# Kernel optimization log

Measured on AMD Instinct MI355X. Metric: run time of the kernel, lower is better.

The kernel has to match this reference:

```python
import jax, jax.numpy as jnp
import numpy as np

N_NODES = 50000
N_EDGES = 640000
WIDTH = 128
K = 5
N_CONVS = 6  # 1 input + 4 hidden + 1 output ChebConv layers


def setup_inputs() -> dict:
    key = jax.random.key(0)
    k1, k2, k3, k4 = jax.random.split(key, 4)
    scale = 1.0 / np.sqrt(WIDTH)
    x = jax.random.normal(k1, (N_NODES, WIDTH), dtype=jnp.float32)
    edge_index = jax.random.randint(k2, (2, N_EDGES), 0, N_NODES, dtype=jnp.int64)
    conv_w = jax.random.normal(k3, (N_CONVS, K, WIDTH, WIDTH), dtype=jnp.float32) * scale
    conv_b = jnp.zeros((N_CONVS, WIDTH), dtype=jnp.float32)
    lin_w = jax.random.normal(k4, (WIDTH, 1), dtype=jnp.float32) * scale
    lin_b = jnp.zeros((1,), dtype=jnp.float32)
    return {"x": x, "edge_index": edge_index, "conv_w": conv_w,
            "conv_b": conv_b, "lin_w": lin_w, "lin_b": lin_b}


def _cheb_norm(edge_index):
    # PyG ChebConv with normalization='sym', lambda_max=2.0:
    # L_hat = 2/lambda_max * (I - D^-1/2 A D^-1/2) - I = -D^-1/2 A D^-1/2
    # (diagonal terms cancel), so per-edge weight = -d_i^-1/2 * d_j^-1/2.
    src, dst = edge_index[0], edge_index[1]
    ones = jnp.ones((edge_index.shape[1],), dtype=jnp.float32)
    deg = jax.ops.segment_sum(ones, dst, num_segments=N_NODES)
    d_inv_sqrt = jnp.where(deg > 0, jax.lax.rsqrt(jnp.maximum(deg, 1e-12)), 0.0)
    return -d_inv_sqrt[src] * d_inv_sqrt[dst]


def _propagate(x, src, dst, norm):
    # L_hat @ x via gather -> weight -> scatter-add
    msg = norm[:, None] * x[src]              # [E, C]
    return jax.ops.segment_sum(msg, dst, num_segments=N_NODES)


def _cheb_conv(x, W, b, src, dst, norm):
    # Chebyshev recurrence: T0=x, T1=Lx, Tk = 2*L*T(k-1) - T(k-2)
    Tx0 = x
    out = Tx0 @ W[0]
    Tx1 = _propagate(Tx0, src, dst, norm)
    out = out + Tx1 @ W[1]
    for k in range(2, K):
        Tx2 = 2.0 * _propagate(Tx1, src, dst, norm) - Tx0
        out = out + Tx2 @ W[k]
        Tx0, Tx1 = Tx1, Tx2
    return out + b


def reference(x, edge_index, conv_w, conv_b, lin_w, lin_b):
    src, dst = edge_index[0], edge_index[1]
    norm = _cheb_norm(edge_index)
    h = x
    # first 5 convs followed by ReLU (dropout is identity in eval mode)
    for l in range(N_CONVS - 1):
        h = _cheb_conv(h, conv_w[l], conv_b[l], src, dst, norm)
        h = jax.nn.relu(h)
    # final conv (no activation) + Linear(128, 1)
    h = _cheb_conv(h, conv_w[N_CONVS - 1], conv_b[N_CONVS - 1], src, dst, norm)
    return h @ lin_w + lin_b
```

## Files before the change

### kernel.cpp

```cpp
#include <hip/hip_runtime.h>


#define NN 50000
#define NE 640000
#define WID 128
#define PROP_BLOCKS 2048

typedef __attribute__((ext_vector_type(8))) short bf16x8;
typedef __attribute__((ext_vector_type(4))) float f32x4;

__device__ __forceinline__ unsigned short f2bf(float f) {
  union { float f; unsigned int u; } v; v.f = f;
  unsigned int r = v.u + 0x7FFF + ((v.u >> 16) & 1);
  return (unsigned short)(r >> 16);
}
__device__ __forceinline__ unsigned int pack2(float lo, float hi) {
  return (unsigned int)f2bf(lo) | ((unsigned int)f2bf(hi) << 16);
}
__device__ __forceinline__ float bflo(unsigned int u) {
  return __uint_as_float(u << 16);
}
__device__ __forceinline__ float bfhi(unsigned int u) {
  return __uint_as_float(u & 0xffff0000u);
}
__device__ __forceinline__ float dec_norm(unsigned int p) {
  unsigned int lo = p & 0xfffu;
  float v = -__uint_as_float(((112u + ((p >> 8) & 15u)) << 23) | ((p & 255u) << 15));
  return (lo == 0u) ? 0.f : v;
}


__global__ __launch_bounds__(256) void degree_kernel(const int* __restrict__ ei,
                                                     int* __restrict__ deg, int E) {
  int e = blockIdx.x * 256 + threadIdx.x;
  if (e < E) atomicAdd(&deg[ei[E + e]], 1);
}

__global__ __launch_bounds__(256) void scan1_kernel(const int* __restrict__ deg,
                                                    int* __restrict__ lex,
                                                    int* __restrict__ bsum,
                                                    float* __restrict__ dinv, int n) {
  __shared__ int ws[4];
  int tid = threadIdx.x, lane = tid & 63, w = tid >> 6;
  int i = blockIdx.x * 256 + tid;
  int cnt = (i < n) ? deg[i] : 0;
  if (i < n) {
    float d = (float)cnt;
    dinv[i] = d > 0.0f ? rsqrtf(d) : 0.0f;
  }
  int v = cnt;
#pragma unroll
  for (int off = 1; off < 64; off <<= 1) {
    int u = __shfl_up(v, off, 64);
    if (lane >= off) v += u;
  }
  if (lane == 63) ws[w] = v;
  __syncthreads();
  int wexcl = 0;
#pragma unroll
  for (int k = 0; k < 4; ++k) wexcl += (k < w) ? ws[k] : 0;
  if (i < n) lex[i] = wexcl + v - cnt;
  if (tid == 255) bsum[blockIdx.x] = wexcl + v;
}

__global__ __launch_bounds__(256) void scan2_kernel(const int* __restrict__ bsum,
                                                    int* __restrict__ boff,
                                                    int* __restrict__ row_end, int nb) {
  __shared__ int ws[4];
  int tid = threadIdx.x, lane = tid & 63, w = tid >> 6;
  int cnt = (tid < nb) ? bsum[tid] : 0;
  int v = cnt;
#pragma unroll
  for (int off = 1; off < 64; off <<= 1) {
    int u = __shfl_up(v, off, 64);
    if (lane >= off) v += u;
  }
  if (lane == 63) ws[w] = v;
  __syncthreads();
  int wexcl = 0;
#pragma unroll
  for (int k = 0; k < 4; ++k) wexcl += (k < w) ? ws[k] : 0;
  if (tid < nb) boff[tid] = wexcl + v - cnt;
  if (tid == 255) *row_end = wexcl + v;
}

__global__ __launch_bounds__(256) void scan3_kernel(const int* __restrict__ lex,
                                                    const int* __restrict__ boff,
                                                    int* __restrict__ row_start,
                                                    int* __restrict__ fill_ptr, int n) {
  int i = blockIdx.x * 256 + threadIdx.x;
  if (i < n) {
    int rs = lex[i] + boff[blockIdx.x];
    row_start[i] = rs;
    fill_ptr[i] = rs;
  }
}

__global__ __launch_bounds__(256) void fill_kernel(const int* __restrict__ ei,
                                                   const float* __restrict__ dinv,
                                                   int* __restrict__ fill_ptr,
                                                   unsigned int* __restrict__ csr, int E) {
  int e = blockIdx.x * 256 + threadIdx.x;
  if (e < E) {
    int s = ei[e];
    int d = ei[E + e];
    int pos = atomicAdd(&fill_ptr[d], 1);
    float mag = dinv[s] * dinv[d];
    unsigned int bits = __float_as_uint(mag);
    unsigned int pk = (unsigned int)s << 12;
    if (bits != 0u) {
      bits += 0x4000u;
      int ex = (int)((bits >> 23) & 255u) - 112;
      ex = max(0, min(15, ex));
      pk |= ((unsigned int)ex << 8) | ((bits >> 15) & 0xffu);
    }
    csr[pos] = pk;
  }
}

__global__ __launch_bounds__(256) void cvt_kernel(const float* __restrict__ x,
                                                  unsigned short* __restrict__ xo,
                                                  const float* __restrict__ w,
                                                  unsigned short* __restrict__ wt,
                                                  int nx, int nw) {
  int i = blockIdx.x * 256 + threadIdx.x;
  if (i < nx) {
    xo[i] = f2bf(x[i]);
  } else if (i < nx + nw) {
    int j = i - nx;
    int l = j / (WID * 640);
    int r = j % (WID * 640);
    int col = r / 640;
    int k = r % 640;
    int kk = k >> 7, m = k & 127;
    wt[j] = f2bf(w[(((size_t)l * 5 + kk) * WID + m) * WID + col]);
  }
}

__global__ __launch_bounds__(256) void vk_kernel(const float* __restrict__ w,
                                                 const float* __restrict__ b,
                                                 const float* __restrict__ lw,
                                                 const float* __restrict__ lb,
                                                 float* __restrict__ V,
                                                 float* __restrict__ cst) {
  int idx = blockIdx.x * 256 + threadIdx.x;
  if (idx < 5 * WID) {
    int k = idx / WID, i = idx % WID;
    const float4* wr = (const float4*)(w + (((size_t)5 * 5 + k) * WID + i) * WID);
    const float4* l4 = (const float4*)lw;
    float s = 0.f;
#pragma unroll 8
    for (int j = 0; j < WID / 4; ++j) {
      float4 a = wr[j], c = l4[j];
      s += a.x * c.x + a.y * c.y + a.z * c.z + a.w * c.w;
    }
    V[idx] = s;
  }
  if (blockIdx.x == 0 && threadIdx.x == 0) {
    float s = 0.f;
    for (int c = 0; c < WID; ++c) s += b[5 * WID + c] * lw[c];
    *cst = s + lb[0];
  }
}


__global__ __launch_bounds__(256) void prop_kernel(unsigned short* __restrict__ out,
                                                   const unsigned short* __restrict__ xin,
                                                   const unsigned short* __restrict__ sub,
                                                   float scale,
                                                   const int* __restrict__ row_start,
                                                   const unsigned int* __restrict__ csr,
                                                   int n) {
  int t = threadIdx.x & 15;
  for (int node = blockIdx.x * 16 + (threadIdx.x >> 4); node < n;
       node += PROP_BLOCKS * 16) {
    int s = row_start[node], e = row_start[node + 1];
    float a0 = 0.f, a1 = 0.f, a2 = 0.f, a3 = 0.f;
    float a4 = 0.f, a5 = 0.f, a6 = 0.f, a7 = 0.f;
    for (int base = s; base < e; base += 16) {
      int cnt = min(16, e - base);
      unsigned int ed = (t < cnt) ? csr[base + t] : 0u;
      int j = 0;
      for (; j + 4 <= cnt; j += 4) {
        unsigned int p0 = (unsigned int)__shfl((int)ed, j, 16);
        unsigned int p1 = (unsigned int)__shfl((int)ed, j + 1, 16);
        unsigned int p2 = (unsigned int)__shfl((int)ed, j + 2, 16);
        unsigned int p3 = (unsigned int)__shfl((int)ed, j + 3, 16);
        int s0 = p0 >> 12, s1 = p1 >> 12, s2 = p2 >> 12, s3 = p3 >> 12;
        float n0 = dec_norm(p0), n1 = dec_norm(p1), n2 = dec_norm(p2), n3 = dec_norm(p3);
        const uint4 v0 = *(const uint4*)(xin + (size_t)s0 * WID + t * 8);
        const uint4 v1 = *(const uint4*)(xin + (size_t)s1 * WID + t * 8);
        const uint4 v2 = *(const uint4*)(xin + (size_t)s2 * WID + t * 8);
        const uint4 v3 = *(const uint4*)(xin + (size_t)s3 * WID + t * 8);
        a0 += n0 * bflo(v0.x) + n1 * bflo(v1.x) + n2 * bflo(v2.x) + n3 * bflo(v3.x);
        a1 += n0 * bfhi(v0.x) + n1 * bfhi(v1.x) + n2 * bfhi(v2.x) + n3 * bfhi(v3.x);
        a2 += n0 * bflo(v0.y) + n1 * bflo(v1.y) + n2 * bflo(v2.y) + n3 * bflo(v3.y);
        a3 += n0 * bfhi(v0.y) + n1 * bfhi(v1.y) + n2 * bfhi(v2.y) + n3 * bfhi(v3.y);
        a4 += n0 * bflo(v0.z) + n1 * bflo(v1.z) + n2 * bflo(v2.z) + n3 * bflo(v3.z);
        a5 += n0 * bfhi(v0.z) + n1 * bfhi(v1.z) + n2 * bfhi(v2.z) + n3 * bfhi(v3.z);
        a6 += n0 * bflo(v0.w) + n1 * bflo(v1.w) + n2 * bflo(v2.w) + n3 * bflo(v3.w);
        a7 += n0 * bfhi(v0.w) + n1 * bfhi(v1.w) + n2 * bfhi(v2.w) + n3 * bfhi(v3.w);
      }
      for (; j < cnt; ++j) {
        unsigned int pj = (unsigned int)__shfl((int)ed, j, 16);
        int sj = pj >> 12;
        float nj = dec_norm(pj);
        const uint4 v = *(const uint4*)(xin + (size_t)sj * WID + t * 8);
        a0 += nj * bflo(v.x); a1 += nj * bfhi(v.x);
        a2 += nj * bflo(v.y); a3 += nj * bfhi(v.y);
        a4 += nj * bflo(v.z); a5 += nj * bfhi(v.z);
        a6 += nj * bflo(v.w); a7 += nj * bfhi(v.w);
      }
    }
    size_t o = (size_t)node * WID + t * 8;
    float r0 = scale * a0, r1 = scale * a1, r2 = scale * a2, r3 = scale * a3;
    float r4 = scale * a4, r5 = scale * a5, r6 = scale * a6, r7 = scale * a7;
    if (sub) {
      const uint4 sv = *(const uint4*)(sub + o);
      r0 -= bflo(sv.x); r1 -= bfhi(sv.x);
      r2 -= bflo(sv.y); r3 -= bfhi(sv.y);
      r4 -= bflo(sv.z); r5 -= bfhi(sv.z);
      r6 -= bflo(sv.w); r7 -= bfhi(sv.w);
    }
    uint4 wv;
    wv.x = pack2(r0, r1); wv.y = pack2(r2, r3);
    wv.z = pack2(r4, r5); wv.w = pack2(r6, r7);
    *(uint4*)(out + o) = wv;
  }
}

__global__ __launch_bounds__(256) void final_proj(const unsigned short* __restrict__ H,
                                                  const float* __restrict__ V,
                                                  const float* __restrict__ cstp,
                                                  float* __restrict__ U,
                                                  float* __restrict__ y, int n) {
  int t = threadIdx.x & 15;
  int node = blockIdx.x * 16 + (threadIdx.x >> 4);
  if (node >= n) return;
  const uint4 h = *(const uint4*)(H + (size_t)node * WID + t * 8);
  float hv0 = bflo(h.x), hv1 = bfhi(h.x), hv2 = bflo(h.y), hv3 = bfhi(h.y);
  float hv4 = bflo(h.z), hv5 = bfhi(h.z), hv6 = bflo(h.w), hv7 = bfhi(h.w);
  float p[5];
#pragma unroll
  for (int k = 0; k < 5; ++k) {
    const float4* vp = (const float4*)(V + k * WID + t * 8);
    float4 v0 = vp[0], v1 = vp[1];
    float s = hv0 * v0.x + hv1 * v0.y + hv2 * v0.z + hv3 * v0.w +
              hv4 * v1.x + hv5 * v1.y + hv6 * v1.z + hv7 * v1.w;
#pragma unroll
    for (int off = 1; off < 16; off <<= 1) s += __shfl_xor(s, off, 16);
    p[k] = s;
  }
  if (t == 0) {
    float4 u0 = {p[0], p[1], p[2], p[3]};
    float4 u1 = {p[4], 0.f, 0.f, 0.f};
    *(float4*)(U + (size_t)node * 8) = u0;
    *(float4*)(U + (size_t)node * 8 + 4) = u1;
    y[node] = p[0] + *cstp;
  }
}

__global__ __launch_bounds__(256) void prop_small(float* __restrict__ out,
                                                  const float* __restrict__ xin,
                                                  const float* __restrict__ sub,
                                                  float scale, int pick,
                                                  float* __restrict__ y,
                                                  const int* __restrict__ row_start,
                                                  const unsigned int* __restrict__ csr,
                                                  int n) {
  int node = blockIdx.x * 256 + threadIdx.x;
  if (node >= n) return;
  int s = row_start[node], e = row_start[node + 1];
  float a0 = 0.f, a1 = 0.f, a2 = 0.f, a3 = 0.f;
  float a4 = 0.f, a5 = 0.f, a6 = 0.f, a7 = 0.f;
  for (int i = s; i < e; ++i) {
    unsigned int p = csr[i];
    int src = (int)(p >> 12);
    float nv = dec_norm(p);
    const float4* r = (const float4*)(xin + (size_t)src * 8);
    float4 v0 = r[0], v1 = r[1];
    a0 += nv * v0.x; a1 += nv * v0.y; a2 += nv * v0.z; a3 += nv * v0.w;
    a4 += nv * v1.x; a5 += nv * v1.y; a6 += nv * v1.z; a7 += nv * v1.w;
  }
  float o0 = scale * a0, o1 = scale * a1, o2 = scale * a2, o3 = scale * a3;
  float o4 = scale * a4, o5 = scale * a5, o6 = scale * a6, o7 = scale * a7;
  if (sub) {
    const float4* sv = (const float4*)(sub + (size_t)node * 8);
    float4 s0 = sv[0], s1 = sv[1];
    o0 -= s0.x; o1 -= s0.y; o2 -= s0.z; o3 -= s0.w;
    o4 -= s1.x; o5 -= s1.y; o6 -= s1.z; o7 -= s1.w;
  }
  float4 w0 = {o0, o1, o2, o3};
  float4 w1 = {o4, o5, o6, o7};
  *(float4*)(out + (size_t)node * 8) = w0;
  *(float4*)(out + (size_t)node * 8 + 4) = w1;
  float yp = o1;
  if (pick == 2) yp = o2;
  if (pick == 3) yp = o3;
  if (pick == 4) yp = o4;
  y[node] += yp;
}


__global__ __launch_bounds__(512) void cheb_gemm(
    const unsigned short* __restrict__ T0, const unsigned short* __restrict__ T1,
    const unsigned short* __restrict__ T2, const unsigned short* __restrict__ T3,
    const unsigned short* __restrict__ T4,
    const unsigned short* __restrict__ Wt,
    const float* __restrict__ bias,
    unsigned short* __restrict__ Hb, int M) {
  __shared__ unsigned short As[128][72];
  __shared__ unsigned short Bs[128][72];
  const unsigned short* chunks[5] = {T0, T1, T2, T3, T4};
  int tid = threadIdx.x;
  int wave = tid >> 6, lane = tid & 63;
  int lrow = lane & 15, quad = lane >> 4;
  int rowBase = blockIdx.x * 128;

  f32x4 acc[8];
#pragma unroll
  for (int b = 0; b < 8; ++b) acc[b] = (f32x4){0.f, 0.f, 0.f, 0.f};

  int ar = tid >> 2, aseg = (tid & 3) * 16;
  int agrow = min(rowBase + ar, M - 1);
  int bc = tid >> 2, bseg = (tid & 3) * 16;

  int4 aR0, aR1, bR0, bR1;
  {
    const unsigned short* ap = chunks[0] + (size_t)agrow * WID + aseg;
    aR0 = *(const int4*)ap;
    aR1 = *(const int4*)(ap + 8);
    const unsigned short* bp = Wt + (size_t)bc * 640 + bseg;
    bR0 = *(const int4*)bp;
    bR1 = *(const int4*)(bp + 8);
  }

  for (int kc = 0; kc < 10; ++kc) {
    *(int4*)(&As[ar][aseg]) = aR0;
    *(int4*)(&As[ar][aseg + 8]) = aR1;
    *(int4*)(&Bs[bc][bseg]) = bR0;
    *(int4*)(&Bs[bc][bseg + 8]) = bR1;
    __syncthreads();

    if (kc < 9) {
      int kn = kc + 1;
      const unsigned short* ap =
          chunks[kn >> 1] + (size_t)agrow * WID + (kn & 1) * 64 + aseg;
      aR0 = *(const int4*)ap;
      aR1 = *(const int4*)(ap + 8);
      const unsigned short* bp = Wt + (size_t)bc * 640 + kn * 64 + bseg;
      bR0 = *(const int4*)bp;
      bR1 = *(const int4*)(bp + 8);
    }

    bf16x8 a0 = *(bf16x8*)(&As[wave * 16 + lrow][quad * 8]);
    bf16x8 a1 = *(bf16x8*)(&As[wave * 16 + lrow][32 + quad * 8]);
#pragma unroll
    for (int ct = 0; ct < 8; ++ct) {
      bf16x8 b0 = *(bf16x8*)(&Bs[ct * 16 + lrow][quad * 8]);
      acc[ct] = __builtin_amdgcn_mfma_f32_16x16x32_bf16(a0, b0, acc[ct], 0, 0, 0);
      bf16x8 b1 = *(bf16x8*)(&Bs[ct * 16 + lrow][32 + quad * 8]);
      acc[ct] = __builtin_amdgcn_mfma_f32_16x16x32_bf16(a1, b1, acc[ct], 0, 0, 0);
    }
    __syncthreads();
  }

#pragma unroll
  for (int ct = 0; ct < 8; ++ct) {
    int gcol = ct * 16 + lrow;
    float bv = bias[gcol];
#pragma unroll
    for (int reg = 0; reg < 4; ++reg) {
      int grow = rowBase + wave * 16 + quad * 4 + reg;
      if (grow < M) {
        float v = fmaxf(acc[ct][reg] + bv, 0.f);
        Hb[(size_t)grow * WID + gcol] = f2bf(v);
      }
    }
  }
}


extern "C" void kernel_launch(void* const* d_in, const int* in_sizes, int n_in,
                              void* d_out, int out_size, void* d_ws, size_t ws_size,
                              hipStream_t stream) {
  const float* x = (const float*)d_in[0];
  const int* ei = (const int*)d_in[1];
  const float* conv_w = (const float*)d_in[2];
  const float* conv_b = (const float*)d_in[3];
  const float* lin_w = (const float*)d_in[4];
  const float* lin_b = (const float*)d_in[5];

  const int N = NN, E = NE, C = WID, L = 6;
  const int NB = (N + 255) / 256;

  char* ws = (char*)d_ws;
  size_t off = 0;
  auto alloc = [&](size_t bytes) -> void* {
    void* p = ws + off;
    off = (off + bytes + 255) & ~(size_t)255;
    return p;
  };
  int* deg = (int*)alloc((size_t)N * 4);
  float* dinv = (float*)alloc((size_t)N * 4);
  int* row_start = (int*)alloc((size_t)(N + 1) * 4);
  int* fill_ptr = (int*)alloc((size_t)N * 4);
  int* lex = (int*)alloc((size_t)N * 4);
  int* bsum = (int*)alloc((size_t)NB * 4);
  int* boff = (int*)alloc((size_t)NB * 4);
  unsigned int* csr = (unsigned int*)alloc((size_t)E * 4);
  unsigned short* Xbf = (unsigned short*)alloc((size_t)N * C * 2);
  unsigned short* Hb0 = (unsigned short*)alloc((size_t)N * C * 2);
  unsigned short* Hb1 = (unsigned short*)alloc((size_t)N * C * 2);
  unsigned short* T1b = (unsigned short*)alloc((size_t)N * C * 2);
  unsigned short* T2b = (unsigned short*)alloc((size_t)N * C * 2);
  unsigned short* T3b = (unsigned short*)alloc((size_t)N * C * 2);
  unsigned short* T4b = (unsigned short*)alloc((size_t)N * C * 2);
  unsigned short* Wt = (unsigned short*)alloc((size_t)5 * C * 640 * 2);
  float* V = (float*)alloc((size_t)5 * C * 4);
  float* cst = (float*)alloc(4);

  hipMemsetAsync(deg, 0, (size_t)N * 4, stream);
  degree_kernel<<<(E + 255) / 256, 256, 0, stream>>>(ei, deg, E);
  scan1_kernel<<<NB, 256, 0, stream>>>(deg, lex, bsum, dinv, N);
  scan2_kernel<<<1, 256, 0, stream>>>(bsum, boff, &row_start[N], NB);
  scan3_kernel<<<NB, 256, 0, stream>>>(lex, boff, row_start, fill_ptr, N);
  fill_kernel<<<(E + 255) / 256, 256, 0, stream>>>(ei, dinv, fill_ptr, csr, E);
  {
    int nx = N * C, nw = 5 * C * 640;
    cvt_kernel<<<(nx + nw + 255) / 256, 256, 0, stream>>>(x, Xbf, conv_w, Wt, nx, nw);
  }
  vk_kernel<<<3, 256, 0, stream>>>(conv_w, conv_b, lin_w, lin_b, V, cst);

  const int gg = (N + 127) / 128;

  for (int l = 0; l < 5; ++l) {
    const unsigned short* T0 = (l == 0) ? Xbf : ((l & 1) ? Hb0 : Hb1);
    unsigned short* Hb = (l & 1) ? Hb1 : Hb0;

    prop_kernel<<<PROP_BLOCKS, 256, 0, stream>>>(T1b, T0, nullptr, 1.0f, row_start, csr, N);
    prop_kernel<<<PROP_BLOCKS, 256, 0, stream>>>(T2b, T1b, T0, 2.0f, row_start, csr, N);
    prop_kernel<<<PROP_BLOCKS, 256, 0, stream>>>(T3b, T2b, T1b, 2.0f, row_start, csr, N);
    prop_kernel<<<PROP_BLOCKS, 256, 0, stream>>>(T4b, T3b, T2b, 2.0f, row_start, csr, N);
    cheb_gemm<<<gg, 512, 0, stream>>>(T0, T1b, T2b, T3b, T4b,
                                      Wt + (size_t)l * C * 640, conv_b + (size_t)l * C,
                                      Hb, N);
  }

  {
    float* y = (float*)d_out;
    float* U  = (float*)T1b;
    float* P1 = (float*)T2b;
    float* P2 = (float*)T3b;
    float* P3 = (float*)T4b;
    float* P4 = (float*)Xbf;
    const int pg = (N + 255) / 256;
    final_proj<<<(N + 15) / 16, 256, 0, stream>>>(Hb0, V, cst, U, y, N);
    prop_small<<<pg, 256, 0, stream>>>(P1, U, nullptr, 1.0f, 1, y, row_start, csr, N);
    prop_small<<<pg, 256, 0, stream>>>(P2, P1, U, 2.0f, 2, y, row_start, csr, N);
    prop_small<<<pg, 256, 0, stream>>>(P3, P2, P1, 2.0f, 3, y, row_start, csr, N);
    prop_small<<<pg, 256, 0, stream>>>(P4, P3, P2, 2.0f, 4, y, row_start, csr, N);
  }
}
```

Before: 838.6 us.

## Partition propagation feature columns across XCD pairs for L2 locality

Rewrites the prop kernel's work split so each group of 4 lanes handles one 32-column quarter of a node row. The quarter is chosen from the block's XCD index (blockIdx & 7), so each pair of XCDs only gathers its own column slice of the source features. The goal is to shrink each XCD's L2 working set for the random gathers and raise cache hit rates. In exchange, each edge index and norm is read four times, the 16-byte-per-lane gathers are narrower per node, and the mapping assumes round-robin dispatch of blocks to 8 XCDs with PROP_BLOCKS equal to 2048.

```diff
diff --git a/kernel.cpp b/kernel.cpp
--- a/kernel.cpp
+++ b/kernel.cpp
@@ -171,27 +171,31 @@
                                                    const int* __restrict__ row_start,
                                                    const unsigned int* __restrict__ csr,
                                                    int n) {
-  int t = threadIdx.x & 15;
-  for (int node = blockIdx.x * 16 + (threadIdx.x >> 4); node < n;
-       node += PROP_BLOCKS * 16) {
+  int t = threadIdx.x & 3;
+  int slot = threadIdx.x >> 2;
+  int xcd = blockIdx.x & 7;
+  int q = xcd >> 1;
+  int r = ((blockIdx.x >> 3) << 1) | (xcd & 1);
+  int co = q * 32 + t * 8;
+
+  for (int node = r * 64 + slot; node < n; node += 512 * 64) {
     int s = row_start[node], e = row_start[node + 1];
     float a0 = 0.f, a1 = 0.f, a2 = 0.f, a3 = 0.f;
     float a4 = 0.f, a5 = 0.f, a6 = 0.f, a7 = 0.f;
-    for (int base = s; base < e; base += 16) {
-      int cnt = min(16, e - base);
+    for (int base = s; base < e; base += 4) {
+      int cnt = min(4, e - base);
       unsigned int ed = (t < cnt) ? csr[base + t] : 0u;
-      int j = 0;
-      for (; j + 4 <= cnt; j += 4) {
-        unsigned int p0 = (unsigned int)__shfl((int)ed, j, 16);
-        unsigned int p1 = (unsigned int)__shfl((int)ed, j + 1, 16);
-        unsigned int p2 = (unsigned int)__shfl((int)ed, j + 2, 16);
-        unsigned int p3 = (unsigned int)__shfl((int)ed, j + 3, 16);
+      if (cnt == 4) {
+        unsigned int p0 = (unsigned int)__shfl((int)ed, 0, 4);
+        unsigned int p1 = (unsigned int)__shfl((int)ed, 1, 4);
+        unsigned int p2 = (unsigned int)__shfl((int)ed, 2, 4);
+        unsigned int p3 = (unsigned int)__shfl((int)ed, 3, 4);
         int s0 = p0 >> 12, s1 = p1 >> 12, s2 = p2 >> 12, s3 = p3 >> 12;
         float n0 = dec_norm(p0), n1 = dec_norm(p1), n2 = dec_norm(p2), n3 = dec_norm(p3);
-        const uint4 v0 = *(const uint4*)(xin + (size_t)s0 * WID + t * 8);
-        const uint4 v1 = *(const uint4*)(xin + (size_t)s1 * WID + t * 8);
-        const uint4 v2 = *(const uint4*)(xin + (size_t)s2 * WID + t * 8);
-        const uint4 v3 = *(const uint4*)(xin + (size_t)s3 * WID + t * 8);
+        const uint4 v0 = *(const uint4*)(xin + (size_t)s0 * WID + co);
+        const uint4 v1 = *(const uint4*)(xin + (size_t)s1 * WID + co);
+        const uint4 v2 = *(const uint4*)(xin + (size_t)s2 * WID + co);
+        const uint4 v3 = *(const uint4*)(xin + (size_t)s3 * WID + co);
         a0 += n0 * bflo(v0.x) + n1 * bflo(v1.x) + n2 * bflo(v2.x) + n3 * bflo(v3.x);
         a1 += n0 * bfhi(v0.x) + n1 * bfhi(v1.x) + n2 * bfhi(v2.x) + n3 * bfhi(v3.x);
         a2 += n0 * bflo(v0.y) + n1 * bflo(v1.y) + n2 * bflo(v2.y) + n3 * bflo(v3.y);
@@ -200,19 +204,20 @@
         a5 += n0 * bfhi(v0.z) + n1 * bfhi(v1.z) + n2 * bfhi(v2.z) + n3 * bfhi(v3.z);
         a6 += n0 * bflo(v0.w) + n1 * bflo(v1.w) + n2 * bflo(v2.w) + n3 * bflo(v3.w);
         a7 += n0 * bfhi(v0.w) + n1 * bfhi(v1.w) + n2 * bfhi(v2.w) + n3 * bfhi(v3.w);
+      } else {
+        for (int j = 0; j < cnt; ++j) {
+          unsigned int pj = (unsigned int)__shfl((int)ed, j, 4);
+          int sj = pj >> 12;
+          float nj = dec_norm(pj);
+          const uint4 v = *(const uint4*)(xin + (size_t)sj * WID + co);
+          a0 += nj * bflo(v.x); a1 += nj * bfhi(v.x);
+          a2 += nj * bflo(v.y); a3 += nj * bfhi(v.y);
+          a4 += nj * bflo(v.z); a5 += nj * bfhi(v.z);
+          a6 += nj * bflo(v.w); a7 += nj * bfhi(v.w);
+        }
       }
-      for (; j < cnt; ++j) {
-        unsigned int pj = (unsigned int)__shfl((int)ed, j, 16);
-        int sj = pj >> 12;
-        float nj = dec_norm(pj);
-        const uint4 v = *(const uint4*)(xin + (size_t)sj * WID + t * 8);
-        a0 += nj * bflo(v.x); a1 += nj * bfhi(v.x);
-        a2 += nj * bflo(v.y); a3 += nj * bfhi(v.y);
-        a4 += nj * bflo(v.z); a5 += nj * bfhi(v.z);
-        a6 += nj * bflo(v.w); a7 += nj * bfhi(v.w);
-      }
-    }
-    size_t o = (size_t)node * WID + t * 8;
+    }
+    size_t o = (size_t)node * WID + co;
     float r0 = scale * a0, r1 = scale * a1, r2 = scale * a2, r3 = scale * a3;
     float r4 = scale * a4, r5 = scale * a5, r6 = scale * a6, r7 = scale * a7;
     if (sub) {
```

Result: slower. 1.089 ms (+29.9%).
